# Performance work log

Measured on AMD Instinct MI355X. Metric: run time of the kernel, lower is better.

The kernel has to match this reference:

```python
import jax, jax.numpy as jnp
import numpy as np

D_IN = 1024
D_OUT = 1024

def setup_inputs() -> dict:
    key = jax.random.key(0)
    kx, kq, kk, kv = jax.random.split(key, 4)
    X = jax.random.normal(kx, (4, 2048, D_IN), dtype=jnp.float32)
    s = 1.0 / np.sqrt(D_IN)
    Wq = jax.random.uniform(kq, (D_IN, D_OUT), jnp.float32, -s, s)
    Wk = jax.random.uniform(kk, (D_IN, D_OUT), jnp.float32, -s, s)
    Wv = jax.random.uniform(kv, (D_IN, D_OUT), jnp.float32, -s, s)
    return {"X": X, "Wq": Wq, "Wk": Wk, "Wv": Wv}

def reference(X, Wq, Wk, Wv):
    # X: [b, s, d_in]; W*: [d_in, d_out] (torch Linear weight transposed)
    B, S, _ = X.shape
    q = jnp.einsum('bsd,de->bse', X, Wq)
    k = jnp.einsum('bsd,de->bse', X, Wk)
    v = jnp.einsum('bsd,de->bse', X, Wv)
    scores = jnp.einsum('bqe,bke->bqk', q, k)  # [b, s, s]
    causal = jnp.triu(jnp.ones((S, S), dtype=bool), k=1)
    scores = jnp.where(causal, -jnp.inf, scores)
    weights = jax.nn.softmax(scores / jnp.sqrt(jnp.asarray(k.shape[-1], scores.dtype)), axis=-1)
    # dropout p=0.0 (eval) -> identity
    return jnp.einsum('bqk,bke->bqe', weights, v)
```

## Files before the change

kernel.cpp:

```cpp
#include <hip/hip_runtime.h>
#include <cstdint>
#include <cmath>

typedef unsigned short u16;
typedef u16   u16x4  __attribute__((ext_vector_type(4)));
typedef u16   u16x8  __attribute__((ext_vector_type(8)));
typedef __bf16 bf16x8 __attribute__((ext_vector_type(8)));
typedef float f32x4  __attribute__((ext_vector_type(4)));

__device__ __forceinline__ u16 f2bf(float f) {
    uint32_t u = __builtin_bit_cast(uint32_t, f);
    u += 0x7fffu + ((u >> 16) & 1u);
    return (u16)(u >> 16);
}
__device__ __forceinline__ float bf2f(u16 v) {
    uint32_t u = ((uint32_t)v) << 16;
    return __builtin_bit_cast(float, u);
}
__device__ __forceinline__ void gload_lds16(const u16* g, u16* l) {
    __builtin_amdgcn_global_load_lds((const __attribute__((address_space(1))) void*)g,
                                     (__attribute__((address_space(3))) void*)l,
                                     16, 0, 0);
}

__global__ __launch_bounds__(256) void prep_kernel(const float* __restrict__ X,
                                                   const float* __restrict__ Wq,
                                                   const float* __restrict__ Wk,
                                                   const float* __restrict__ Wv,
                                                   u16* __restrict__ Xb,
                                                   u16* __restrict__ Wt) {
    __shared__ u16 tile[64 * 72];
    typedef float f4 __attribute__((ext_vector_type(4)));
    const int bid = blockIdx.x;
    if (bid < 8192) {
        const int idx = bid * 256 + threadIdx.x;
        f4 f = ((const f4*)X)[idx];
        u16x4 o;
        o[0] = f2bf(f[0]); o[1] = f2bf(f[1]); o[2] = f2bf(f[2]); o[3] = f2bf(f[3]);
        ((u16x4*)Xb)[idx] = o;
        return;
    }
    const int id = bid - 8192;
    const int z = id >> 8, rem = id & 255;
    const float* W = (z == 0) ? Wq : (z == 1) ? Wk : Wv;
    u16* out = Wt + ((size_t)z << 20);
    const int nt = (rem & 15) * 64, kt = (rem >> 4) * 64;
    const int t = threadIdx.x, r = t >> 2, cq = (t & 3) * 16;
    const float* src = W + (size_t)(kt + r) * 1024 + nt + cq;
#pragma unroll
    for (int q = 0; q < 4; q++) {
        f4 f = ((const f4*)src)[q];
        tile[r * 72 + cq + q * 4 + 0] = f2bf(f[0]);
        tile[r * 72 + cq + q * 4 + 1] = f2bf(f[1]);
        tile[r * 72 + cq + q * 4 + 2] = f2bf(f[2]);
        tile[r * 72 + cq + q * 4 + 3] = f2bf(f[3]);
    }
    __syncthreads();
    u16x8 o0, o1;
#pragma unroll
    for (int e = 0; e < 8; e++) { o0[e] = tile[(cq + e) * 72 + r]; o1[e] = tile[(cq + 8 + e) * 72 + r]; }
    u16* dst = out + (size_t)(nt + r) * 1024 + kt + cq;
    *(u16x8*)dst = o0;
    *(u16x8*)(dst + 8) = o1;
}

template <int OUTMODE>
__device__ __forceinline__ void gemm_bt_core(u16* __restrict__ smem,
                                             const u16* __restrict__ A,
                                             const u16* __restrict__ Bt,
                                             void* __restrict__ outp,
                                             const int ldk, const int ldo,
                                             const int kbeg, const int kend,
                                             const int m0, const int n0,
                                             const int om0, const int on0) {
    u16* As = smem;
    u16* Bs = smem + 4096;
    const int tid = (int)threadIdx.x;
    const int wave = tid >> 6, lane = tid & 63;
    const int wm = wave >> 1, wn = wave & 1;

    f32x4 acc[4][4] = {};

    const int sr = lane >> 2;
    const int scw = ((lane & 3) ^ ((sr >> 1) & 3)) * 8;
    const u16* gA = A  + (size_t)(m0 + wave * 32 + sr) * ldk + scw;
    const u16* gB = Bt + (size_t)(n0 + wave * 32 + sr) * ldk + scw;
    u16* lA = As + wave * 1024;
    u16* lB = Bs + wave * 1024;
    const size_t rstep = (size_t)ldk * 16;

    const int arow = lane & 15;
    const int ksw  = (arow >> 1) & 3;
    const int koff = (((lane >> 4) ^ ksw)) * 8;
    const u16* pa = As + (wm * 64 + arow) * 32 + koff;
    const u16* pb = Bs + (wn * 64 + arow) * 32 + koff;

    for (int k0 = kbeg; k0 < kend; k0 += 32) {
        gload_lds16(gA + k0,         lA);
        gload_lds16(gA + k0 + rstep, lA + 512);
        gload_lds16(gB + k0,         lB);
        gload_lds16(gB + k0 + rstep, lB + 512);
        __syncthreads();
        bf16x8 a[4], b[4];
#pragma unroll
        for (int i = 0; i < 4; i++) a[i] = *(const bf16x8*)(pa + i * 512);
#pragma unroll
        for (int j = 0; j < 4; j++) b[j] = *(const bf16x8*)(pb + j * 512);
#pragma unroll
        for (int i = 0; i < 4; i++)
#pragma unroll
            for (int j = 0; j < 4; j++)
                acc[i][j] = __builtin_amdgcn_mfma_f32_16x16x32_bf16(a[i], b[j], acc[i][j], 0, 0, 0);
        __syncthreads();
    }

    const int row0 = om0 + wm * 64 + ((lane >> 4) << 2);
    const int col0 = on0 + wn * 64 + (lane & 15);
    if constexpr (OUTMODE == 0) {
        u16* o = (u16*)outp;
#pragma unroll
        for (int i = 0; i < 4; i++)
#pragma unroll
            for (int r = 0; r < 4; r++) {
                u16* po = o + (size_t)(row0 + i * 16 + r) * ldo + col0;
#pragma unroll
                for (int j = 0; j < 4; j++) po[j * 16] = f2bf(acc[i][j][r]);
            }
    } else {
        float* o = (float*)outp;
#pragma unroll
        for (int i = 0; i < 4; i++)
#pragma unroll
            for (int r = 0; r < 4; r++) {
                float* po = o + (size_t)(row0 + i * 16 + r) * ldo + col0;
#pragma unroll
                for (int j = 0; j < 4; j++) po[j * 16] = acc[i][j][r];
            }
    }
}

__global__ __launch_bounds__(512, 2) void qkv_gemm_kernel(const u16* __restrict__ Xb,
                                                          const u16* __restrict__ Wt,
                                                          u16* __restrict__ QKV) {
    __shared__ u16 lds[65536];
    const int bid = blockIdx.x;
    const int xcd = bid & 7, slot = bid >> 3;
    const int z = slot >> 4, r16 = slot & 15;
    const int m0 = (xcd * 4 + (r16 >> 2)) << 8;
    const int n0 = (r16 & 3) << 8;

    const u16* __restrict__ A = Xb;
    const u16* __restrict__ B = Wt + ((size_t)z << 20);
    u16* __restrict__ C = QKV + ((size_t)z << 23);

    const int tid = (int)threadIdx.x;
    const int w = tid >> 6, l = tid & 63;
    const int wm = w >> 2, wn = w & 3;

    const int srow = w * 16 + (l >> 3);
    const int scol = ((l & 7) ^ ((l >> 3) & 7)) * 8;
    const u16* gA = A + (size_t)(m0 + srow) * 1024 + scol;
    const u16* gB = B + (size_t)(n0 + srow) * 1024 + scol;
    u16* const sA = lds + w * 1024;
    u16* const sB = lds + 32768 + w * 1024;

    const int c0 = ((l >> 4) ^ (l & 7)) * 8;
    const u16* const pa_ = lds + (wm * 64 + (l & 15)) * 64;
    const u16* const pb_ = lds + 32768 + (wn * 32 + (l & 15)) * 64;

    f32x4 acc[2][2][4][2] = {};
    bf16x8 a[4][2], b0[2][2], b1[2][2];

#define MFMA_ __builtin_amdgcn_mfma_f32_16x16x32_bf16
#define STG_A(BUF, H, T) \
    gload_lds16(gA + (size_t)((H) * 128) * 1024 + (T) * 64,       sA + (BUF) + (H) * 8192); \
    gload_lds16(gA + (size_t)((H) * 128 + 8) * 1024 + (T) * 64,   sA + (BUF) + (H) * 8192 + 512);
#define STG_B(BUF, H, T) \
    gload_lds16(gB + (size_t)((H) * 128) * 1024 + (T) * 64,       sB + (BUF) + (H) * 8192); \
    gload_lds16(gB + (size_t)((H) * 128 + 8) * 1024 + (T) * 64,   sB + (BUF) + (H) * 8192 + 512);
#define LD_A(BUF, QA) \
    _Pragma("unroll") for (int m_ = 0; m_ < 4; m_++) { \
        a[m_][0] = *(const bf16x8*)(pa_ + (BUF) + (QA) * 8192 + m_ * 1024 + c0); \
        a[m_][1] = *(const bf16x8*)(pa_ + (BUF) + (QA) * 8192 + m_ * 1024 + (c0 ^ 32)); \
    }
#define LD_B(BUF, QB, DST) \
    _Pragma("unroll") for (int n_ = 0; n_ < 2; n_++) { \
        DST[n_][0] = *(const bf16x8*)(pb_ + (BUF) + (QB) * 8192 + n_ * 1024 + c0); \
        DST[n_][1] = *(const bf16x8*)(pb_ + (BUF) + (QB) * 8192 + n_ * 1024 + (c0 ^ 32)); \
    }
#define MM(QA, QB, BV) \
    _Pragma("unroll") for (int m_ = 0; m_ < 4; m_++) { \
        _Pragma("unroll") for (int n_ = 0; n_ < 2; n_++) { \
            acc[QA][QB][m_][n_] = MFMA_(a[m_][0], BV[n_][0], acc[QA][QB][m_][n_], 0, 0, 0); \
            acc[QA][QB][m_][n_] = MFMA_(a[m_][1], BV[n_][1], acc[QA][QB][m_][n_], 0, 0, 0); \
        } \
    }
#define VM6 asm volatile("s_waitcnt vmcnt(6)" ::: "memory");
#define VM0 asm volatile("s_waitcnt vmcnt(0)" ::: "memory");
#define VMN
#define BAR __builtin_amdgcn_s_barrier();
#define PRIO1 __builtin_amdgcn_s_setprio(1);
#define PRIO0 __builtin_amdgcn_s_setprio(0);
#define TILE(BUF, OBUF, T1, S1, T2, S2, VM) \
    LD_A(BUF, 0) LD_B(BUF, 0, b0) \
    if (S1) { STG_A(OBUF, 1, T1) } \
    BAR PRIO1 MM(0, 0, b0) PRIO0 BAR \
    LD_B(BUF, 1, b1) \
    if (S2) { STG_A(BUF, 0, T2) } \
    BAR PRIO1 MM(0, 1, b1) PRIO0 BAR \
    LD_A(BUF, 1) \
    if (S2) { STG_B(BUF, 0, T2) } \
    BAR PRIO1 MM(1, 0, b0) PRIO0 BAR \
    if (S2) { STG_B(BUF, 1, T2) } \
    VM \
    BAR PRIO1 MM(1, 1, b1) PRIO0 BAR

    STG_A(0, 0, 0) STG_B(0, 0, 0) STG_B(0, 1, 0) STG_A(0, 1, 0)
    STG_A(16384, 0, 1) STG_B(16384, 0, 1) STG_B(16384, 1, 1)
    asm volatile("s_waitcnt vmcnt(6)" ::: "memory");
    __builtin_amdgcn_s_barrier();

#pragma unroll 1
    for (int i = 0; i < 7; ++i) {
        const int t1 = 2 * i + 1, t2 = 2 * i + 2, t3 = 2 * i + 3;
        TILE(0,     16384, t1, 1, t2, 1, VM6)
        TILE(16384, 0,     t2, 1, t3, 1, VM6)
    }
    TILE(0,     16384, 15, 1, 0, 0, VM0)
    TILE(16384, 0,     0,  0, 0, 0, VMN)

    const int row0 = m0 + wm * 64 + ((l >> 4) << 2);
    const int col0 = n0 + wn * 32 + (l & 15);
#pragma unroll
    for (int qa = 0; qa < 2; qa++)
#pragma unroll
        for (int qb = 0; qb < 2; qb++)
#pragma unroll
            for (int m = 0; m < 4; m++)
#pragma unroll
                for (int r = 0; r < 4; r++) {
                    u16* po = C + (size_t)(row0 + qa * 128 + m * 16 + r) * 1024 + col0 + qb * 128;
#pragma unroll
                    for (int n = 0; n < 2; n++) po[n * 16] = f2bf(acc[qa][qb][m][n][r]);
                }
#undef MFMA_
#undef STG_A
#undef STG_B
#undef LD_A
#undef LD_B
#undef MM
#undef VM6
#undef VM0
#undef VMN
#undef BAR
#undef PRIO1
#undef PRIO0
#undef TILE
}

__global__ __launch_bounds__(256) void s_tr_kernel(const u16* __restrict__ QKV,
                                                   u16* __restrict__ S,
                                                   u16* __restrict__ Vt) {
    __shared__ u16 smem[8192];
    const int bid = blockIdx.x;
    if (bid < 576) {
        const int xcd = bid & 7, slot = bid >> 3;
        const int b = xcd >> 1, half = xcd & 1;
        int it = half ? 11 : 0;
        const int ntiles = half ? 70 : 66;
        if (slot >= ntiles) return;
        int acc = 0;
        while (acc + it + 1 <= slot) { acc += it + 1; it++; }
        const int jt = slot - acc;
        const u16* Q  = QKV + ((size_t)b << 21);
        const u16* Kp = QKV + ((size_t)1 << 23) + ((size_t)b << 21);
        gemm_bt_core<0>(smem, Q, Kp, S + ((size_t)b << 22), 1024, 2048, 0, 1024,
                        it * 128, jt * 128, it * 128, jt * 128);
        return;
    }
    const int id = bid - 576;
    const int z = id >> 9, rem = id & 511;
    const u16* src = QKV + ((size_t)2 << 23) + ((size_t)z << 21);
    u16* dst = Vt + ((size_t)z << 21);
    const int st = (rem & 31) * 64, et = (rem >> 5) * 64;
    u16 (*tile)[72] = (u16(*)[72])smem;
    const int t = threadIdx.x, r = t >> 2, cq = (t & 3) * 16;
    const u16* p = src + (size_t)(st + r) * 1024 + et + cq;
    u16x8 u0 = *(const u16x8*)p;
    u16x8 u1 = *(const u16x8*)(p + 8);
#pragma unroll
    for (int e = 0; e < 8; e++) { tile[r][cq + e] = u0[e]; tile[r][cq + 8 + e] = u1[e]; }
    __syncthreads();
    u16x8 o0, o1;
#pragma unroll
    for (int e = 0; e < 8; e++) { o0[e] = tile[cq + e][r]; o1[e] = tile[cq + 8 + e][r]; }
    u16* q = dst + (size_t)(et + r) * 2048 + st + cq;
    *(u16x8*)q = o0;
    *(u16x8*)(q + 8) = o1;
}

__global__ __launch_bounds__(256) void pv_gemm_kernel(const u16* __restrict__ P,
                                                      const u16* __restrict__ Vt,
                                                      float* __restrict__ O,
                                                      float* __restrict__ Part) {
    __shared__ u16 smem[8192];
    const unsigned char IT[24]   = {15,14, 7,14,13,13,12,12, 15, 6,11,11,10,10, 9, 5,  0, 1, 2, 8, 3, 9, 8, 4};
    const unsigned char KIND[24] = { 1, 1, 0, 2, 1, 2, 1, 2,  2, 0, 1, 2, 1, 2, 1, 0,  0, 0, 0, 2, 0, 2, 1, 0};
    const int j = blockIdx.x;
    const int slot = j >> 5, combo = j & 31;
    const int it = IT[slot], kind = KIND[slot];
    const int b = combo >> 3, n0 = (combo & 7) * 128;
    const int u = it + 1, h = (u + 1) >> 1;
    const int k_lo = (kind == 2) ? h * 128 : 0;
    const int k_hi = (kind == 1) ? h * 128 : u * 128;
    if (kind == 2) {
        float* dst = Part + ((size_t)((it - 8) * 32 + combo) << 14);
        gemm_bt_core<1>(smem, P + ((size_t)b << 22), Vt + ((size_t)b << 21), dst,
                        2048, 128, k_lo, k_hi, it * 128, n0, 0, 0);
    } else {
        gemm_bt_core<1>(smem, P + ((size_t)b << 22), Vt + ((size_t)b << 21),
                        O + ((size_t)b << 21),
                        2048, 1024, k_lo, k_hi, it * 128, n0, it * 128, n0);
    }
}

__global__ __launch_bounds__(256) void reduce_kernel(float* __restrict__ O,
                                                     const float* __restrict__ Part) {
    const int t = blockIdx.x;
    const int tile = t >> 2, q = t & 3;
    const int it = 8 + (tile >> 5), combo = tile & 31;
    const int b = combo >> 3, n0 = (combo & 7) * 128;
    const f32x4* p = (const f32x4*)(Part + ((size_t)tile << 14)) + q * 1024;
    float* o = O + ((size_t)b << 21) + (size_t)(it * 128 + q * 32) * 1024 + n0;
    const int tid = threadIdx.x;
#pragma unroll
    for (int e = 0; e < 4; e++) {
        const int flat = e * 256 + tid;
        const int row = flat >> 5, col = (flat & 31) * 4;
        f32x4 pv = p[flat];
        f32x4* po = (f32x4*)(o + (size_t)row * 1024 + col);
        f32x4 ov = *po;
        ov[0] += pv[0]; ov[1] += pv[1]; ov[2] += pv[2]; ov[3] += pv[3];
        *po = ov;
    }
}

__global__ __launch_bounds__(256) void softmax_kernel(u16* __restrict__ S) {
    const int wave = threadIdx.x >> 6, lane = threadIdx.x & 63;
    const int g = blockIdx.x * 4 + wave;
    const int b = g >> 11, i = g & 2047;
    u16* row = S + ((size_t)b << 22) + ((size_t)i << 11);
    const int n = i + 1;
    const int kend = ((i >> 7) + 1) << 7;
    const int nt_ = (kend + 511) >> 9;
    const float NEG = -1e30f;
    float v[32];
    float m = NEG;
#pragma unroll
    for (int t = 0; t < 4; t++) {
        if (t < nt_) {
            u16x8 u = *(const u16x8*)(row + t * 512 + lane * 8);
#pragma unroll
            for (int e = 0; e < 8; e++) {
                const int col = t * 512 + lane * 8 + e;
                float f = (col < n) ? bf2f(u[e]) : NEG;
                v[t * 8 + e] = f;
                m = fmaxf(m, f);
            }
        }
    }
#pragma unroll
    for (int off = 32; off > 0; off >>= 1) m = fmaxf(m, __shfl_xor(m, off, 64));
    const float sc = 0.03125f * 1.44269504088896f;
    float s = 0.f;
#pragma unroll
    for (int t = 0; t < 4; t++) {
        if (t < nt_) {
#pragma unroll
            for (int e = 0; e < 8; e++) {
                const float x = v[t * 8 + e];
                const float e2 = (x == NEG) ? 0.f : exp2f((x - m) * sc);
                v[t * 8 + e] = e2;
                s += e2;
            }
        }
    }
#pragma unroll
    for (int off = 32; off > 0; off >>= 1) s += __shfl_xor(s, off, 64);
    const float inv = 1.f / s;
#pragma unroll
    for (int t = 0; t < 4; t++) {
        if (t < nt_) {
            u16x8 o;
#pragma unroll
            for (int e = 0; e < 8; e++) o[e] = f2bf(v[t * 8 + e] * inv);
            *(u16x8*)(row + t * 512 + lane * 8) = o;
        }
    }
}

extern "C" void kernel_launch(void* const* d_in, const int* in_sizes, int n_in,
                              void* d_out, int out_size, void* d_ws, size_t ws_size,
                              hipStream_t stream) {
    const float* X  = (const float*)d_in[0];
    const float* Wq = (const float*)d_in[1];
    const float* Wk = (const float*)d_in[2];
    const float* Wv = (const float*)d_in[3];
    float* out = (float*)d_out;

    u16* ws  = (u16*)d_ws;
    u16* Xb  = ws;
    u16* Wt  = Xb + ((size_t)1 << 23);
    u16* QKV = Wt + 3 * ((size_t)1 << 20);
    u16* S   = QKV + 3 * ((size_t)1 << 23);
    u16* Vt  = Xb;
    float* Part = (float*)QKV;

    prep_kernel<<<8960, 256, 0, stream>>>(X, Wq, Wk, Wv, Xb, Wt);
    qkv_gemm_kernel<<<384, 512, 0, stream>>>(Xb, Wt, QKV);
    s_tr_kernel<<<2624, 256, 0, stream>>>(QKV, S, Vt);
    softmax_kernel<<<2048, 256, 0, stream>>>(S);
    pv_gemm_kernel<<<768, 256, 0, stream>>>(S, Vt, out, Part);
    reduce_kernel<<<1024, 256, 0, stream>>>(out, Part);
}
```

Before: 237.6 us.

## Shrink QKV GEMM block tile to 256x128 and double grid size

The QKV projection GEMM drops from a 256x256 to a 256x128 output tile per block, launching 768 blocks instead of 384. The B staging, LDS footprint, accumulators and pipeline wait counts are restructured to match. This aims to fill more CUs (384 blocks on 256 CUs leaves an uneven tail) and cut registers and LDS per block. The cost is lower arithmetic intensity per block and more reloads of the A tile from global memory.

```diff
diff --git a/kernel.cpp b/kernel.cpp
--- a/kernel.cpp
+++ b/kernel.cpp
@@ -142,12 +142,12 @@
 __global__ __launch_bounds__(512, 2) void qkv_gemm_kernel(const u16* __restrict__ Xb,
                                                           const u16* __restrict__ Wt,
                                                           u16* __restrict__ QKV) {
-    __shared__ u16 lds[65536];
+    __shared__ u16 lds[49152];
     const int bid = blockIdx.x;
     const int xcd = bid & 7, slot = bid >> 3;
-    const int z = slot >> 4, r16 = slot & 15;
-    const int m0 = (xcd * 4 + (r16 >> 2)) << 8;
-    const int n0 = (r16 & 3) << 8;
+    const int z = slot >> 5, r32 = slot & 31;
+    const int m0 = (xcd * 4 + (r32 >> 3)) << 8;
+    const int n0 = (r32 & 7) << 7;
 
     const u16* __restrict__ A = Xb;
     const u16* __restrict__ B = Wt + ((size_t)z << 20);
@@ -168,81 +168,74 @@
     const u16* const pa_ = lds + (wm * 64 + (l & 15)) * 64;
     const u16* const pb_ = lds + 32768 + (wn * 32 + (l & 15)) * 64;
 
-    f32x4 acc[2][2][4][2] = {};
-    bf16x8 a[4][2], b0[2][2], b1[2][2];
+    f32x4 acc[2][4][2] = {};
+    bf16x8 a[4][2], b[2][2];
 
 #define MFMA_ __builtin_amdgcn_mfma_f32_16x16x32_bf16
 #define STG_A(BUF, H, T) \
     gload_lds16(gA + (size_t)((H) * 128) * 1024 + (T) * 64,       sA + (BUF) + (H) * 8192); \
     gload_lds16(gA + (size_t)((H) * 128 + 8) * 1024 + (T) * 64,   sA + (BUF) + (H) * 8192 + 512);
-#define STG_B(BUF, H, T) \
-    gload_lds16(gB + (size_t)((H) * 128) * 1024 + (T) * 64,       sB + (BUF) + (H) * 8192); \
-    gload_lds16(gB + (size_t)((H) * 128 + 8) * 1024 + (T) * 64,   sB + (BUF) + (H) * 8192 + 512);
+#define STG_B(BUF, T) \
+    gload_lds16(gB + (T) * 64,                                    sB + ((BUF) >> 1)); \
+    gload_lds16(gB + (size_t)8 * 1024 + (T) * 64,                 sB + ((BUF) >> 1) + 512);
 #define LD_A(BUF, QA) \
     _Pragma("unroll") for (int m_ = 0; m_ < 4; m_++) { \
         a[m_][0] = *(const bf16x8*)(pa_ + (BUF) + (QA) * 8192 + m_ * 1024 + c0); \
         a[m_][1] = *(const bf16x8*)(pa_ + (BUF) + (QA) * 8192 + m_ * 1024 + (c0 ^ 32)); \
     }
-#define LD_B(BUF, QB, DST) \
+#define LD_B(BUF) \
     _Pragma("unroll") for (int n_ = 0; n_ < 2; n_++) { \
-        DST[n_][0] = *(const bf16x8*)(pb_ + (BUF) + (QB) * 8192 + n_ * 1024 + c0); \
-        DST[n_][1] = *(const bf16x8*)(pb_ + (BUF) + (QB) * 8192 + n_ * 1024 + (c0 ^ 32)); \
-    }
-#define MM(QA, QB, BV) \
+        b[n_][0] = *(const bf16x8*)(pb_ + ((BUF) >> 1) + n_ * 1024 + c0); \
+        b[n_][1] = *(const bf16x8*)(pb_ + ((BUF) >> 1) + n_ * 1024 + (c0 ^ 32)); \
+    }
+#define MM(QA) \
     _Pragma("unroll") for (int m_ = 0; m_ < 4; m_++) { \
         _Pragma("unroll") for (int n_ = 0; n_ < 2; n_++) { \
-            acc[QA][QB][m_][n_] = MFMA_(a[m_][0], BV[n_][0], acc[QA][QB][m_][n_], 0, 0, 0); \
-            acc[QA][QB][m_][n_] = MFMA_(a[m_][1], BV[n_][1], acc[QA][QB][m_][n_], 0, 0, 0); \
+            acc[QA][m_][n_] = MFMA_(a[m_][0], b[n_][0], acc[QA][m_][n_], 0, 0, 0); \
+            acc[QA][m_][n_] = MFMA_(a[m_][1], b[n_][1], acc[QA][m_][n_], 0, 0, 0); \
         } \
     }
 #define VM6 asm volatile("s_waitcnt vmcnt(6)" ::: "memory");
+#define VM2 asm volatile("s_waitcnt vmcnt(2)" ::: "memory");
 #define VM0 asm volatile("s_waitcnt vmcnt(0)" ::: "memory");
 #define VMN
 #define BAR __builtin_amdgcn_s_barrier();
 #define PRIO1 __builtin_amdgcn_s_setprio(1);
 #define PRIO0 __builtin_amdgcn_s_setprio(0);
-#define TILE(BUF, OBUF, T1, S1, T2, S2, VM) \
-    LD_A(BUF, 0) LD_B(BUF, 0, b0) \
+#define TILE(BUF, OBUF, T1, S1, T2, S2, VMA, VMB) \
+    LD_A(BUF, 0) LD_B(BUF) \
     if (S1) { STG_A(OBUF, 1, T1) } \
-    BAR PRIO1 MM(0, 0, b0) PRIO0 BAR \
-    LD_B(BUF, 1, b1) \
-    if (S2) { STG_A(BUF, 0, T2) } \
-    BAR PRIO1 MM(0, 1, b1) PRIO0 BAR \
+    VMA BAR PRIO1 MM(0) PRIO0 BAR \
     LD_A(BUF, 1) \
-    if (S2) { STG_B(BUF, 0, T2) } \
-    BAR PRIO1 MM(1, 0, b0) PRIO0 BAR \
-    if (S2) { STG_B(BUF, 1, T2) } \
-    VM \
-    BAR PRIO1 MM(1, 1, b1) PRIO0 BAR
-
-    STG_A(0, 0, 0) STG_B(0, 0, 0) STG_B(0, 1, 0) STG_A(0, 1, 0)
-    STG_A(16384, 0, 1) STG_B(16384, 0, 1) STG_B(16384, 1, 1)
+    if (S2) { STG_A(BUF, 0, T2) STG_B(BUF, T2) } \
+    VMB BAR PRIO1 MM(1) PRIO0 BAR
+
+    STG_A(0, 0, 0) STG_B(0, 0) STG_A(0, 1, 0)
+    STG_A(16384, 0, 1) STG_B(16384, 1)
     asm volatile("s_waitcnt vmcnt(6)" ::: "memory");
     __builtin_amdgcn_s_barrier();
 
 #pragma unroll 1
     for (int i = 0; i < 7; ++i) {
         const int t1 = 2 * i + 1, t2 = 2 * i + 2, t3 = 2 * i + 3;
-        TILE(0,     16384, t1, 1, t2, 1, VM6)
-        TILE(16384, 0,     t2, 1, t3, 1, VM6)
-    }
-    TILE(0,     16384, 15, 1, 0, 0, VM0)
-    TILE(16384, 0,     0,  0, 0, 0, VMN)
+        TILE(0,     16384, t1, 1, t2, 1, VM6, VM6)
+        TILE(16384, 0,     t2, 1, t3, 1, VM6, VM6)
+    }
+    TILE(0,     16384, 15, 1, 0, 0, VM6, VM2)
+    TILE(16384, 0,     0,  0, 0, 0, VM0, VMN)
 
     const int row0 = m0 + wm * 64 + ((l >> 4) << 2);
     const int col0 = n0 + wn * 32 + (l & 15);
 #pragma unroll
     for (int qa = 0; qa < 2; qa++)
 #pragma unroll
-        for (int qb = 0; qb < 2; qb++)
-#pragma unroll
-            for (int m = 0; m < 4; m++)
-#pragma unroll
-                for (int r = 0; r < 4; r++) {
-                    u16* po = C + (size_t)(row0 + qa * 128 + m * 16 + r) * 1024 + col0 + qb * 128;
-#pragma unroll
-                    for (int n = 0; n < 2; n++) po[n * 16] = f2bf(acc[qa][qb][m][n][r]);
-                }
+        for (int m = 0; m < 4; m++)
+#pragma unroll
+            for (int r = 0; r < 4; r++) {
+                u16* po = C + (size_t)(row0 + qa * 128 + m * 16 + r) * 1024 + col0;
+#pragma unroll
+                for (int n = 0; n < 2; n++) po[n * 16] = f2bf(acc[qa][m][n][r]);
+            }
 #undef MFMA_
 #undef STG_A
 #undef STG_B
@@ -250,6 +243,7 @@
 #undef LD_B
 #undef MM
 #undef VM6
+#undef VM2
 #undef VM0
 #undef VMN
 #undef BAR
@@ -417,7 +411,7 @@
     float* Part = (float*)QKV;
 
     prep_kernel<<<8960, 256, 0, stream>>>(X, Wq, Wk, Wv, Xb, Wt);
-    qkv_gemm_kernel<<<384, 512, 0, stream>>>(Xb, Wt, QKV);
+    qkv_gemm_kernel<<<768, 512, 0, stream>>>(Xb, Wt, QKV);
     s_tr_kernel<<<2624, 256, 0, stream>>>(QKV, S, Vt);
     softmax_kernel<<<2048, 256, 0, stream>>>(S);
     pv_gemm_kernel<<<768, 256, 0, stream>>>(S, Vt, out, Part);
```

Result: no change. 237.6 us (+0.0%).
